# Kernel optimization log

Hardware: AMD Instinct MI355X
Metric: run time of the kernel (lower is better)

## Reference

```python
import jax, jax.numpy as jnp
import numpy as np

N = 100000
E = 1600000
IN_FEATS = 256
OUT_FEATS = 64


def setup_inputs() -> dict:
    key = jax.random.key(0)
    k1, k2, k3, k4, k5, k6 = jax.random.split(key, 6)
    X = jax.random.normal(k1, (N, IN_FEATS), dtype=jnp.float32)
    edge_row = jax.random.randint(k2, (E,), 0, N, dtype=jnp.int32)
    edge_col = jax.random.randint(k3, (E,), 0, N, dtype=jnp.int32)
    # normalized adjacency values (A_hat entries), positive like D^-1/2 A D^-1/2
    edge_vals = jax.random.uniform(k4, (E,), dtype=jnp.float32)
    stdv = 1.0 / np.sqrt(OUT_FEATS)
    W = jax.random.uniform(k5, (IN_FEATS, OUT_FEATS), dtype=jnp.float32,
                           minval=-stdv, maxval=stdv)
    b = jax.random.uniform(k6, (OUT_FEATS,), dtype=jnp.float32,
                           minval=-stdv, maxval=stdv)
    return {"X": X, "edge_row": edge_row, "edge_col": edge_col,
            "edge_vals": edge_vals, "W": W, "b": b}


def reference(X, edge_row, edge_col, edge_vals, W, b):
    # Dense GEMM: [N, in] @ [in, out] -> [N, out]
    XW = X @ W
    # SpMM: out[r] = sum_{e: row[e]==r} vals[e] * XW[col[e]]
    msgs = edge_vals[:, None] * XW[edge_col]          # [E, out]
    out = jax.ops.segment_sum(msgs, edge_row, num_segments=X.shape[0])
    out = out + b
    return jax.nn.relu(out)
```

## Files before the change

### kernel.cpp

```cpp
#include <hip/hip_runtime.h>

#define K_IN 256
#define N_OUT 64

__global__ __launch_bounds__(256) void gemm_xw(const float* __restrict__ X,
                                               const float* __restrict__ W,
                                               float* __restrict__ XW, int n) {
  __shared__ float Xs[64][68];
  __shared__ float Ws[64][68];
  const int tid = threadIdx.x;
  const int row0 = blockIdx.x * 64;
  const int tx = tid & 15;
  const int ty = tid >> 4;
  float acc[4][4] = {};
  for (int kc = 0; kc < K_IN; kc += 64) {
#pragma unroll
    for (int i = 0; i < 4; ++i) {
      int flat = tid + i * 256;
      int r = flat >> 4;
      int q = flat & 15;
      int gr = row0 + r; if (gr >= n) gr = n - 1;
      float4 xv = *reinterpret_cast<const float4*>(&X[(size_t)gr * K_IN + kc + q * 4]);
      *reinterpret_cast<float4*>(&Xs[r][q * 4]) = xv;
      float4 wv = *reinterpret_cast<const float4*>(&W[(size_t)(kc + r) * N_OUT + q * 4]);
      *reinterpret_cast<float4*>(&Ws[r][q * 4]) = wv;
    }
    __syncthreads();
#pragma unroll
    for (int k = 0; k < 64; ++k) {
      float4 wv = *reinterpret_cast<const float4*>(&Ws[k][tx * 4]);
#pragma unroll
      for (int i = 0; i < 4; ++i) {
        float xv = Xs[ty * 4 + i][k];
        acc[i][0] += xv * wv.x;
        acc[i][1] += xv * wv.y;
        acc[i][2] += xv * wv.z;
        acc[i][3] += xv * wv.w;
      }
    }
    __syncthreads();
  }
#pragma unroll
  for (int i = 0; i < 4; ++i) {
    int gr = row0 + ty * 4 + i;
    if (gr < n) {
      float4 o = make_float4(acc[i][0], acc[i][1], acc[i][2], acc[i][3]);
      *reinterpret_cast<float4*>(&XW[(size_t)gr * N_OUT + tx * 4]) = o;
    }
  }
}

__global__ void hist_rows(const int* __restrict__ er, int* __restrict__ cnt, int E) {
  int i = blockIdx.x * blockDim.x + threadIdx.x;
  if (i < E) atomicAdd(&cnt[er[i]], 1);
}

__global__ void scan_blocks(const int* __restrict__ cnt, int* __restrict__ offs,
                            int* __restrict__ partials, int n) {
  __shared__ int sd[2][256];
  int tid = threadIdx.x;
  int base = blockIdx.x * 1024 + tid * 4;
  int v[4]; int s = 0;
#pragma unroll
  for (int i = 0; i < 4; ++i) {
    int idx = base + i;
    int c = (idx < n) ? cnt[idx] : 0;
    v[i] = s; s += c;
  }
  int buf = 0; sd[0][tid] = s; __syncthreads();
#pragma unroll
  for (int d = 1; d < 256; d <<= 1) {
    int x = sd[buf][tid];
    if (tid >= d) x += sd[buf][tid - d];
    sd[buf ^ 1][tid] = x; buf ^= 1; __syncthreads();
  }
  int texcl = (tid > 0) ? sd[buf][tid - 1] : 0;
  if (tid == 255) partials[blockIdx.x] = sd[buf][255];
#pragma unroll
  for (int i = 0; i < 4; ++i) {
    int idx = base + i;
    if (idx < n) offs[idx] = texcl + v[i];
  }
}

__global__ void scan_single(const int* __restrict__ in, int* __restrict__ outp, int n) {
  __shared__ int sd[2][256];
  int tid = threadIdx.x;
  int base = tid * 4;
  int v[4]; int s = 0;
#pragma unroll
  for (int i = 0; i < 4; ++i) {
    int idx = base + i;
    int c = (idx < n) ? in[idx] : 0;
    v[i] = s; s += c;
  }
  int buf = 0; sd[0][tid] = s; __syncthreads();
#pragma unroll
  for (int d = 1; d < 256; d <<= 1) {
    int x = sd[buf][tid];
    if (tid >= d) x += sd[buf][tid - d];
    sd[buf ^ 1][tid] = x; buf ^= 1; __syncthreads();
  }
  int texcl = (tid > 0) ? sd[buf][tid - 1] : 0;
#pragma unroll
  for (int i = 0; i < 4; ++i) {
    int idx = base + i;
    if (idx < n) outp[idx] = texcl + v[i];
  }
}

__global__ void finalize_offs(int* __restrict__ offs, int* __restrict__ wp,
                              const int* __restrict__ pp, int n, int E) {
  int i = blockIdx.x * blockDim.x + threadIdx.x;
  if (i < n) {
    int v = offs[i] + pp[i >> 10];
    offs[i] = v; wp[i] = v;
  } else if (i == n) {
    offs[n] = E;
  }
}

__global__ void scatter_edges(const int* __restrict__ er, const int* __restrict__ ec,
                              const float* __restrict__ ev, int* __restrict__ wp,
                              int* __restrict__ ccol, float* __restrict__ cval, int E) {
  int e = blockIdx.x * blockDim.x + threadIdx.x;
  if (e >= E) return;
  int r = er[e];
  int p = atomicAdd(&wp[r], 1);
  ccol[p] = ec[e];
  cval[p] = ev[e];
}

__global__ __launch_bounds__(256) void spmm_rows(const int* __restrict__ offs,
    const int* __restrict__ ccol, const float* __restrict__ cval,
    const float* __restrict__ xw, const float* __restrict__ bias,
    float* __restrict__ out, int n) {
  int wid = (int)((blockIdx.x * blockDim.x + threadIdx.x) >> 6);
  int lane = threadIdx.x & 63;
  if (wid >= n) return;
  int start = offs[wid], end = offs[wid + 1];
  float acc = 0.f;
  for (int e0 = start; e0 < end; e0 += 64) {
    int m = end - e0; if (m > 64) m = 64;
    int c = 0; float v = 0.f;
    if (lane < m) { c = ccol[e0 + lane]; v = cval[e0 + lane]; }
    for (int i = 0; i < m; ++i) {
      int ci = __shfl(c, i);
      float vi = __shfl(v, i);
      acc += vi * xw[(size_t)ci * N_OUT + lane];
    }
  }
  out[(size_t)wid * N_OUT + lane] = fmaxf(acc + bias[lane], 0.f);
}

__global__ void spmm_atomic(const int* __restrict__ er, const int* __restrict__ ec,
                            const float* __restrict__ ev, const float* __restrict__ xw,
                            float* __restrict__ out, int E) {
  int wid = (int)((blockIdx.x * blockDim.x + threadIdx.x) >> 6);
  int lane = threadIdx.x & 63;
  if (wid >= E) return;
  int r = er[wid], c = ec[wid];
  float v = ev[wid];
  atomicAdd(&out[(size_t)r * N_OUT + lane], v * xw[(size_t)c * N_OUT + lane]);
}

__global__ void bias_relu(float* __restrict__ out, const float* __restrict__ bias, int total) {
  int i = blockIdx.x * blockDim.x + threadIdx.x;
  if (i < total) out[i] = fmaxf(out[i] + bias[i & (N_OUT - 1)], 0.f);
}

extern "C" void kernel_launch(void* const* d_in, const int* in_sizes, int n_in,
                              void* d_out, int out_size, void* d_ws, size_t ws_size,
                              hipStream_t stream) {
  const float* X    = (const float*)d_in[0];
  const int*   er   = (const int*)d_in[1];
  const int*   ec   = (const int*)d_in[2];
  const float* ev   = (const float*)d_in[3];
  const float* W    = (const float*)d_in[4];
  const float* bias = (const float*)d_in[5];
  const int n = in_sizes[0] / K_IN;
  const int E = in_sizes[1];
  float* out = (float*)d_out;

  auto rnd = [](size_t b) { return (b + 255) & ~(size_t)255; };
  const size_t sz_xw   = rnd((size_t)n * N_OUT * 4);
  const size_t sz_cnt  = rnd((size_t)n * 4);
  const size_t sz_offs = rnd(((size_t)n + 1) * 4);
  const size_t sz_wp   = sz_cnt;
  const int nb_scan = (n + 1023) / 1024;
  const size_t sz_part = rnd((size_t)nb_scan * 4);
  const size_t sz_col  = rnd((size_t)E * 4);
  const size_t sz_val  = rnd((size_t)E * 4);
  const size_t need = sz_xw + sz_cnt + sz_offs + sz_wp + 2 * sz_part + sz_col + sz_val;

  char* ws = (char*)d_ws;
  float* xw = (float*)ws; ws += sz_xw;

  gemm_xw<<<(n + 63) / 64, 256, 0, stream>>>(X, W, xw, n);

  if (ws_size >= need && nb_scan <= 1024) {
    int*   cnt   = (int*)ws;   ws += sz_cnt;
    int*   offs  = (int*)ws;   ws += sz_offs;
    int*   wp    = (int*)ws;   ws += sz_wp;
    int*   part  = (int*)ws;   ws += sz_part;
    int*   pp    = (int*)ws;   ws += sz_part;
    int*   ccol  = (int*)ws;   ws += sz_col;
    float* cval  = (float*)ws; ws += sz_val;

    hipMemsetAsync(cnt, 0, (size_t)n * 4, stream);
    hist_rows<<<(E + 255) / 256, 256, 0, stream>>>(er, cnt, E);
    scan_blocks<<<nb_scan, 256, 0, stream>>>(cnt, offs, part, n);
    scan_single<<<1, 256, 0, stream>>>(part, pp, nb_scan);
    finalize_offs<<<(n + 1 + 255) / 256, 256, 0, stream>>>(offs, wp, pp, n, E);
    scatter_edges<<<(E + 255) / 256, 256, 0, stream>>>(er, ec, ev, wp, ccol, cval, E);
    spmm_rows<<<(n + 3) / 4, 256, 0, stream>>>(offs, ccol, cval, xw, bias, out, n);
  } else {
    hipMemsetAsync(out, 0, (size_t)n * N_OUT * 4, stream);
    spmm_atomic<<<(E + 3) / 4, 256, 0, stream>>>(er, ec, ev, xw, out, E);
    bias_relu<<<(n * N_OUT + 255) / 256, 256, 0, stream>>>(out, bias, n * N_OUT);
  }
}
```

Baseline: 466.9 us.

## Replace per-row CSR build with bucketed multisplit and shared-memory accumulating SpMM

Drops the full per-row CSR construction (row histogram, multi-level scan, scatter with random global atomics). Edges are now binned into 256-row buckets: a shared-memory bucket histogram, a single-block scan, and a block-local multisplit that writes packed (local row, col, val) records in mostly contiguous runs. A per-bucket SpMM kernel accumulates into a 64KB LDS tile with shared atomics, software-prefetches the gathered XW rows, and fuses bias and ReLU on write-out. This trades global atomic and scatter traffic for LDS atomics and coarse 1024-thread blocks. Only about 391 such blocks are launched, so load balance and occupancy may suffer, and the column is packed into 24 bits.

```diff
diff --git a/kernel.cpp b/kernel.cpp
--- a/kernel.cpp
+++ b/kernel.cpp
@@ -2,6 +2,9 @@
 
 #define K_IN 256
 #define N_OUT 64
+#define RPB 256
+#define MAX_NB 512
+#define MS_CHUNK 4096
 
 __global__ __launch_bounds__(256) void gemm_xw(const float* __restrict__ X,
                                                const float* __restrict__ W,
@@ -50,107 +53,156 @@
   }
 }
 
-__global__ void hist_rows(const int* __restrict__ er, int* __restrict__ cnt, int E) {
-  int i = blockIdx.x * blockDim.x + threadIdx.x;
-  if (i < E) atomicAdd(&cnt[er[i]], 1);
-}
-
-__global__ void scan_blocks(const int* __restrict__ cnt, int* __restrict__ offs,
-                            int* __restrict__ partials, int n) {
-  __shared__ int sd[2][256];
+__global__ __launch_bounds__(256) void bucket_hist(const int* __restrict__ er,
+                                                   int* __restrict__ gh, int E, int NB) {
+  __shared__ int h[MAX_NB];
+  for (int k = threadIdx.x; k < MAX_NB; k += 256) h[k] = 0;
+  __syncthreads();
+  for (int i = blockIdx.x * 256 + threadIdx.x; i < E; i += gridDim.x * 256)
+    atomicAdd(&h[er[i] >> 8], 1);
+  __syncthreads();
+  for (int k = threadIdx.x; k < NB; k += 256)
+    if (h[k]) atomicAdd(&gh[k], h[k]);
+}
+
+__global__ __launch_bounds__(256) void scan_small(const int* __restrict__ gh,
+    int* __restrict__ boffs, int* __restrict__ gwp, int NB, int E) {
+  __shared__ int sc[2][MAX_NB];
   int tid = threadIdx.x;
-  int base = blockIdx.x * 1024 + tid * 4;
-  int v[4]; int s = 0;
-#pragma unroll
-  for (int i = 0; i < 4; ++i) {
-    int idx = base + i;
-    int c = (idx < n) ? cnt[idx] : 0;
-    v[i] = s; s += c;
-  }
-  int buf = 0; sd[0][tid] = s; __syncthreads();
-#pragma unroll
-  for (int d = 1; d < 256; d <<= 1) {
-    int x = sd[buf][tid];
-    if (tid >= d) x += sd[buf][tid - d];
-    sd[buf ^ 1][tid] = x; buf ^= 1; __syncthreads();
-  }
-  int texcl = (tid > 0) ? sd[buf][tid - 1] : 0;
-  if (tid == 255) partials[blockIdx.x] = sd[buf][255];
-#pragma unroll
-  for (int i = 0; i < 4; ++i) {
-    int idx = base + i;
-    if (idx < n) offs[idx] = texcl + v[i];
-  }
-}
-
-__global__ void scan_single(const int* __restrict__ in, int* __restrict__ outp, int n) {
-  __shared__ int sd[2][256];
-  int tid = threadIdx.x;
-  int base = tid * 4;
-  int v[4]; int s = 0;
-#pragma unroll
-  for (int i = 0; i < 4; ++i) {
-    int idx = base + i;
-    int c = (idx < n) ? in[idx] : 0;
-    v[i] = s; s += c;
-  }
-  int buf = 0; sd[0][tid] = s; __syncthreads();
-#pragma unroll
-  for (int d = 1; d < 256; d <<= 1) {
-    int x = sd[buf][tid];
-    if (tid >= d) x += sd[buf][tid - d];
-    sd[buf ^ 1][tid] = x; buf ^= 1; __syncthreads();
-  }
-  int texcl = (tid > 0) ? sd[buf][tid - 1] : 0;
-#pragma unroll
-  for (int i = 0; i < 4; ++i) {
-    int idx = base + i;
-    if (idx < n) outp[idx] = texcl + v[i];
-  }
-}
-
-__global__ void finalize_offs(int* __restrict__ offs, int* __restrict__ wp,
-                              const int* __restrict__ pp, int n, int E) {
-  int i = blockIdx.x * blockDim.x + threadIdx.x;
-  if (i < n) {
-    int v = offs[i] + pp[i >> 10];
-    offs[i] = v; wp[i] = v;
-  } else if (i == n) {
-    offs[n] = E;
-  }
-}
-
-__global__ void scatter_edges(const int* __restrict__ er, const int* __restrict__ ec,
-                              const float* __restrict__ ev, int* __restrict__ wp,
-                              int* __restrict__ ccol, float* __restrict__ cval, int E) {
-  int e = blockIdx.x * blockDim.x + threadIdx.x;
-  if (e >= E) return;
-  int r = er[e];
-  int p = atomicAdd(&wp[r], 1);
-  ccol[p] = ec[e];
-  cval[p] = ev[e];
-}
-
-__global__ __launch_bounds__(256) void spmm_rows(const int* __restrict__ offs,
-    const int* __restrict__ ccol, const float* __restrict__ cval,
+  for (int k = tid; k < MAX_NB; k += 256) sc[0][k] = (k < NB) ? gh[k] : 0;
+  __syncthreads();
+  int buf = 0;
+  for (int d = 1; d < MAX_NB; d <<= 1) {
+    for (int k = tid; k < MAX_NB; k += 256) {
+      int v = sc[buf][k];
+      if (k >= d) v += sc[buf][k - d];
+      sc[buf ^ 1][k] = v;
+    }
+    buf ^= 1; __syncthreads();
+  }
+  for (int k = tid; k < NB; k += 256) {
+    int ex = (k > 0) ? sc[buf][k - 1] : 0;
+    boffs[k] = ex; gwp[k] = ex;
+  }
+  if (tid == 0) boffs[NB] = E;
+}
+
+__global__ __launch_bounds__(256) void multisplit(
+    const int* __restrict__ er, const int* __restrict__ ec,
+    const float* __restrict__ ev, int* __restrict__ gwp,
+    int2* __restrict__ binned, int E) {
+  __shared__ int h[MAX_NB];
+  __shared__ int sc[2][MAX_NB];
+  __shared__ int lsc[MAX_NB];
+  __shared__ int base[MAX_NB];
+  __shared__ int cursor[MAX_NB];
+  __shared__ int2 staged[MS_CHUNK];
+  __shared__ unsigned short sbkt[MS_CHUNK];
+  const int tid = threadIdx.x;
+  const int bb = blockIdx.x * MS_CHUNK;
+
+  for (int k = tid; k < MAX_NB; k += 256) h[k] = 0;
+  __syncthreads();
+
+  int rrow[16]; int rcol[16]; float rval[16];
+#pragma unroll
+  for (int k = 0; k < 16; ++k) {
+    int idx = bb + k * 256 + tid;
+    if (idx < E) {
+      rrow[k] = er[idx]; rcol[k] = ec[idx]; rval[k] = ev[idx];
+      atomicAdd(&h[rrow[k] >> 8], 1);
+    } else rrow[k] = -1;
+  }
+  __syncthreads();
+  for (int k = tid; k < MAX_NB; k += 256) sc[0][k] = h[k];
+  __syncthreads();
+  int buf = 0;
+  for (int d = 1; d < MAX_NB; d <<= 1) {
+    for (int k = tid; k < MAX_NB; k += 256) {
+      int v = sc[buf][k];
+      if (k >= d) v += sc[buf][k - d];
+      sc[buf ^ 1][k] = v;
+    }
+    buf ^= 1; __syncthreads();
+  }
+  for (int k = tid; k < MAX_NB; k += 256) {
+    int ex = (k > 0) ? sc[buf][k - 1] : 0;
+    lsc[k] = ex; cursor[k] = ex;
+    int c = h[k];
+    base[k] = (c > 0) ? atomicAdd(&gwp[k], c) : 0;
+  }
+  __syncthreads();
+#pragma unroll
+  for (int k = 0; k < 16; ++k) {
+    if (rrow[k] >= 0) {
+      int b = rrow[k] >> 8;
+      int pos = atomicAdd(&cursor[b], 1);
+      staged[pos] = make_int2(((rrow[k] & 255) << 24) | rcol[k], __float_as_int(rval[k]));
+      sbkt[pos] = (unsigned short)b;
+    }
+  }
+  __syncthreads();
+  int nv = E - bb; if (nv > MS_CHUNK) nv = MS_CHUNK;
+  for (int s = tid; s < nv; s += 256) {
+    int b = sbkt[s];
+    binned[base[b] + (s - lsc[b])] = staged[s];
+  }
+}
+
+__global__ __launch_bounds__(1024) void bucket_spmm(
+    const int* __restrict__ boffs, const int2* __restrict__ binned,
     const float* __restrict__ xw, const float* __restrict__ bias,
     float* __restrict__ out, int n) {
-  int wid = (int)((blockIdx.x * blockDim.x + threadIdx.x) >> 6);
-  int lane = threadIdx.x & 63;
-  if (wid >= n) return;
-  int start = offs[wid], end = offs[wid + 1];
-  float acc = 0.f;
-  for (int e0 = start; e0 < end; e0 += 64) {
-    int m = end - e0; if (m > 64) m = 64;
-    int c = 0; float v = 0.f;
-    if (lane < m) { c = ccol[e0 + lane]; v = cval[e0 + lane]; }
-    for (int i = 0; i < m; ++i) {
-      int ci = __shfl(c, i);
-      float vi = __shfl(v, i);
-      acc += vi * xw[(size_t)ci * N_OUT + lane];
-    }
-  }
-  out[(size_t)wid * N_OUT + lane] = fmaxf(acc + bias[lane], 0.f);
+  __shared__ float acc[RPB * N_OUT];
+  const int tid = threadIdx.x;
+  const int lane = tid & 63;
+  const int wid = tid >> 6;
+  const int b = blockIdx.x;
+  const int r0 = b * RPB;
+
+  for (int k = tid; k < RPB * N_OUT; k += 1024) acc[k] = 0.f;
+  __syncthreads();
+
+  const int s0 = boffs[b], s1 = boffs[b + 1];
+  const float bv = bias[lane];
+
+  for (int be = s0 + wid * 64; be < s1; be += 16 * 64) {
+    int m = s1 - be; if (m > 64) m = 64;
+    int key = 0; float v = 0.f;
+    if (lane < m) {
+      int2 rec = binned[be + lane];
+      key = rec.x; v = __int_as_float(rec.y);
+    }
+    float pre[8];
+#pragma unroll
+    for (int j = 0; j < 8; ++j) {
+      int c = __shfl(key, j) & 0xFFFFFF;
+      pre[j] = xw[(size_t)c * N_OUT + lane];
+    }
+#pragma unroll
+    for (int i = 0; i < 64; i += 8) {
+#pragma unroll
+      for (int j = 0; j < 8; ++j) {
+        int kk = __shfl(key, i + j);
+        float vv = __shfl(v, i + j);
+        float x = pre[j];
+        if (i + 8 < 64) {
+          int cn = __shfl(key, i + 8 + j) & 0xFFFFFF;
+          pre[j] = xw[(size_t)cn * N_OUT + lane];
+        }
+        int ri = ((unsigned)kk) >> 24;
+        atomicAdd(&acc[ri * N_OUT + lane], vv * x);
+      }
+    }
+  }
+  __syncthreads();
+#pragma unroll
+  for (int k = 0; k < 16; ++k) {
+    int lr = wid + k * 16;
+    int gr = r0 + lr;
+    if (gr < n)
+      out[(size_t)gr * N_OUT + lane] = fmaxf(acc[lr * N_OUT + lane] + bv, 0.f);
+  }
 }
 
 __global__ void spmm_atomic(const int* __restrict__ er, const int* __restrict__ ec,
@@ -182,38 +234,32 @@
   const int E = in_sizes[1];
   float* out = (float*)d_out;
 
+  const int NB = (n + RPB - 1) / RPB;
+
   auto rnd = [](size_t b) { return (b + 255) & ~(size_t)255; };
-  const size_t sz_xw   = rnd((size_t)n * N_OUT * 4);
-  const size_t sz_cnt  = rnd((size_t)n * 4);
-  const size_t sz_offs = rnd(((size_t)n + 1) * 4);
-  const size_t sz_wp   = sz_cnt;
-  const int nb_scan = (n + 1023) / 1024;
-  const size_t sz_part = rnd((size_t)nb_scan * 4);
-  const size_t sz_col  = rnd((size_t)E * 4);
-  const size_t sz_val  = rnd((size_t)E * 4);
-  const size_t need = sz_xw + sz_cnt + sz_offs + sz_wp + 2 * sz_part + sz_col + sz_val;
+  const size_t sz_xw     = rnd((size_t)n * N_OUT * 4);
+  const size_t sz_gh     = rnd((size_t)MAX_NB * 4);
+  const size_t sz_boffs  = rnd((size_t)(MAX_NB + 1) * 4);
+  const size_t sz_gwp    = rnd((size_t)MAX_NB * 4);
+  const size_t sz_binned = rnd((size_t)E * 8);
+  const size_t need = sz_xw + sz_gh + sz_boffs + sz_gwp + sz_binned;
 
   char* ws = (char*)d_ws;
   float* xw = (float*)ws; ws += sz_xw;
 
   gemm_xw<<<(n + 63) / 64, 256, 0, stream>>>(X, W, xw, n);
 
-  if (ws_size >= need && nb_scan <= 1024) {
-    int*   cnt   = (int*)ws;   ws += sz_cnt;
-    int*   offs  = (int*)ws;   ws += sz_offs;
-    int*   wp    = (int*)ws;   ws += sz_wp;
-    int*   part  = (int*)ws;   ws += sz_part;
-    int*   pp    = (int*)ws;   ws += sz_part;
-    int*   ccol  = (int*)ws;   ws += sz_col;
-    float* cval  = (float*)ws; ws += sz_val;
-
-    hipMemsetAsync(cnt, 0, (size_t)n * 4, stream);
-    hist_rows<<<(E + 255) / 256, 256, 0, stream>>>(er, cnt, E);
-    scan_blocks<<<nb_scan, 256, 0, stream>>>(cnt, offs, part, n);
-    scan_single<<<1, 256, 0, stream>>>(part, pp, nb_scan);
-    finalize_offs<<<(n + 1 + 255) / 256, 256, 0, stream>>>(offs, wp, pp, n, E);
-    scatter_edges<<<(E + 255) / 256, 256, 0, stream>>>(er, ec, ev, wp, ccol, cval, E);
-    spmm_rows<<<(n + 3) / 4, 256, 0, stream>>>(offs, ccol, cval, xw, bias, out, n);
+  if (ws_size >= need && NB <= MAX_NB) {
+    int*  gh     = (int*)ws;  ws += sz_gh;
+    int*  boffs  = (int*)ws;  ws += sz_boffs;
+    int*  gwp    = (int*)ws;  ws += sz_gwp;
+    int2* binned = (int2*)ws; ws += sz_binned;
+
+    hipMemsetAsync(gh, 0, (size_t)MAX_NB * 4, stream);
+    bucket_hist<<<512, 256, 0, stream>>>(er, gh, E, NB);
+    scan_small<<<1, 256, 0, stream>>>(gh, boffs, gwp, NB, E);
+    multisplit<<<(E + MS_CHUNK - 1) / MS_CHUNK, 256, 0, stream>>>(er, ec, ev, gwp, binned, E);
+    bucket_spmm<<<NB, 1024, 0, stream>>>(boffs, binned, xw, bias, out, n);
   } else {
     hipMemsetAsync(out, 0, (size_t)n * N_OUT * 4, stream);
     spmm_atomic<<<(E + 3) / 4, 256, 0, stream>>>(er, ec, ev, xw, out, E);
```

New measurement: 953.9 us. 2.04x slower.
